# Optimization experiments

Measured on AMD Instinct MI355X. Metric: run time of the kernel, lower is better.

## Reference

```python
import jax, jax.numpy as jnp
import numpy as np

NUM_HEADS = 8
LN_EPS = 1e-6


def setup_inputs() -> dict:
    key = jax.random.key(0)
    ks = jax.random.split(key, 10)
    B, H, W, C = 4, 64, 64, 256
    s = 1.0 / np.sqrt(C)
    return {
        "x": jax.random.normal(ks[0], (B, H, W, C), jnp.float32),
        "Wq": jax.random.normal(ks[1], (C, C), jnp.float32) * s,
        "bq": jnp.zeros((C,), jnp.float32),
        "Wk": jax.random.normal(ks[2], (C, C), jnp.float32) * s,
        "bk": jnp.zeros((C,), jnp.float32),
        "Wv": jax.random.normal(ks[3], (C, C), jnp.float32) * s,
        "bv": jnp.zeros((C,), jnp.float32),
        "Wo": jax.random.normal(ks[4], (C, C), jnp.float32) * s,
        "bo": jnp.zeros((C,), jnp.float32),
        "gamma": jnp.ones((C,), jnp.float32),
        "beta": jnp.zeros((C,), jnp.float32),
    }


def reference(x, Wq, bq, Wk, bk, Wv, bv, Wo, bo, gamma, beta):
    B, H, W, C = x.shape
    N = H * W
    nh, dh = NUM_HEADS, C // NUM_HEADS
    xs = x.reshape(B, N, C)
    # torch Linear: y = x @ W.T + b
    q = (xs @ Wq.T + bq).reshape(B, N, nh, dh)
    k = (xs @ Wk.T + bk).reshape(B, N, nh, dh)
    v = (xs @ Wv.T + bv).reshape(B, N, nh, dh)
    residual = v.reshape(B, N, C)  # residual is V, per the original module
    # explicit attention (dropout on logits is identity in eval mode)
    scale = 1.0 / jnp.sqrt(jnp.asarray(dh, x.dtype))
    attn = jnp.einsum('bqhd,bkhd->bhqk', q, k) * scale  # [B, nh, N, N]
    probs = jax.nn.softmax(attn, axis=-1)
    out = jnp.einsum('bhqk,bkhd->bqhd', probs, v).reshape(B, N, C)
    out = out @ Wo.T + bo
    out = out + residual
    # LayerNorm over last dim, eps=1e-6
    mu = jnp.mean(out, axis=-1, keepdims=True)
    var = jnp.mean(jnp.square(out - mu), axis=-1, keepdims=True)
    out = (out - mu) * jax.lax.rsqrt(var + LN_EPS) * gamma + beta
    return out
```

## Files before the change

kernel.cpp:

```cpp
#include <hip/hip_runtime.h>
#include <hip/hip_bf16.h>
#include <math.h>

#define NHD 8
#define DH 32
#define CC 256
#define NTOK 4096
#define BATCH 4
#define MTOT 16384

typedef __attribute__((ext_vector_type(8))) short short8;
typedef __attribute__((ext_vector_type(4))) short s16x4;
typedef __attribute__((ext_vector_type(4))) float f32x4;
typedef __attribute__((ext_vector_type(16))) float f32x16;
typedef __attribute__((ext_vector_type(2))) unsigned int u32x2;

#if __has_builtin(__builtin_amdgcn_exp2f)
#define EXP2F __builtin_amdgcn_exp2f
#else
#define EXP2F exp2f
#endif

__device__ inline float bf2f(short s) {
    unsigned int u = ((unsigned int)(unsigned short)s) << 16;
    float f; __builtin_memcpy(&f, &u, 4); return f;
}
__device__ inline short f2bf(float f) {
    __hip_bfloat16 h = __float2bfloat16(f);
    unsigned short u; __builtin_memcpy(&u, &h, 2); return (short)u;
}
__device__ inline unsigned int pack2(float lo, float hi) {
    unsigned int a = (unsigned short)f2bf(lo);
    unsigned int b = (unsigned short)f2bf(hi);
    return a | (b << 16);
}
__device__ inline short8 mk8(unsigned int a, unsigned int b, unsigned int c, unsigned int d) {
    unsigned int t[4] = {a, b, c, d};
    short8 r; __builtin_memcpy(&r, t, 16); return r;
}

__global__ __launch_bounds__(256) void conv_x_kernel(const float* __restrict__ src,
                                                     short* __restrict__ dst, int n8) {
    int t = blockIdx.x * 256 + threadIdx.x;
    if (t >= n8) return;
    const f32x4* s4 = (const f32x4*)src;
    f32x4 a = s4[t * 2], b = s4[t * 2 + 1];
    short8 o;
    o[0] = f2bf(a[0]); o[1] = f2bf(a[1]); o[2] = f2bf(a[2]); o[3] = f2bf(a[3]);
    o[4] = f2bf(b[0]); o[5] = f2bf(b[1]); o[6] = f2bf(b[2]); o[7] = f2bf(b[3]);
    ((short8*)dst)[t] = o;
}

__global__ __launch_bounds__(256) void conv_w_kernel(const float* __restrict__ Wq,
                                                     const float* __restrict__ Wk,
                                                     const float* __restrict__ Wv,
                                                     const float* __restrict__ Wo,
                                                     short* __restrict__ dst) {
    int w = blockIdx.y;
    const float* src = (w == 0) ? Wq : (w == 1) ? Wk : (w == 2) ? Wv : Wo;
    int t = blockIdx.x * 256 + threadIdx.x;
    const f32x4* s4 = (const f32x4*)src;
    f32x4 a = s4[t * 2], b = s4[t * 2 + 1];
    short8 o;
    o[0] = f2bf(a[0]); o[1] = f2bf(a[1]); o[2] = f2bf(a[2]); o[3] = f2bf(a[3]);
    o[4] = f2bf(b[0]); o[5] = f2bf(b[1]); o[6] = f2bf(b[2]); o[7] = f2bf(b[3]);
    ((short8*)(dst + w * 65536))[t] = o;
}

__global__ __launch_bounds__(256) void qkv_kernel(const short* __restrict__ xb,
                                                  const short* __restrict__ Wb,
                                                  const float* __restrict__ bq,
                                                  const float* __restrict__ bk,
                                                  const float* __restrict__ bv,
                                                  short* __restrict__ Qb,
                                                  short* __restrict__ Kb,
                                                  short* __restrict__ Vt,
                                                  short* __restrict__ Vres) {
    int wsel = blockIdx.y;
    const short* W = Wb + wsel * 65536;
    int wave = threadIdx.x >> 6;
    int lane = threadIdx.x & 63;
    int lo = lane & 15, hi = lane >> 4;
    int m0 = blockIdx.x * 64 + wave * 16;

    f32x4 acc[16];
#pragma unroll
    for (int i = 0; i < 16; i++) acc[i] = (f32x4){0, 0, 0, 0};

    for (int ks = 0; ks < 8; ks++) {
        short8 a = *(const short8*)(xb + (m0 + lo) * 256 + ks * 32 + hi * 8);
#pragma unroll
        for (int nf = 0; nf < 16; nf++) {
            short8 b = *(const short8*)(W + (nf * 16 + lo) * 256 + ks * 32 + hi * 8);
            acc[nf] = __builtin_amdgcn_mfma_f32_16x16x32_bf16(a, b, acc[nf], 0, 0, 0);
        }
    }
    const float* bias = (wsel == 0) ? bq : (wsel == 1) ? bk : bv;
    const float qscale = 0.17677669529663687f * 1.4426950408889634f;
#pragma unroll
    for (int nf = 0; nf < 16; nf++) {
#pragma unroll
        for (int r = 0; r < 4; r++) {
            int m = m0 + hi * 4 + r;
            int c = nf * 16 + lo;
            float v = acc[nf][r] + bias[c];
            int bb = m >> 12, n = m & 4095;
            int h = c >> 5, d = c & 31;
            int bh = bb * 8 + h;
            if (wsel == 0)      Qb[(bh * 4096 + n) * 32 + d] = f2bf(v * qscale);
            else if (wsel == 1) Kb[(bh * 4096 + n) * 32 + d] = f2bf(v);
            else {
                short s = f2bf(v);
                Vt[(bh * 32 + d) * 4096 + n] = s;
                Vres[m * 256 + c] = s;
            }
        }
    }
}

__global__ __launch_bounds__(256, 4) void attn_kernel(const short* __restrict__ Qb,
                                                      const short* __restrict__ Kb,
                                                      const short* __restrict__ Vt,
                                                      short* __restrict__ O) {
    int bx = blockIdx.x;
    int bh = bx >> 5;
    int qb = bx & 31;
    int wave = threadIdx.x >> 6, lane = threadIdx.x & 63;
    int l31 = lane & 31, lh = lane >> 5;
    int q0 = qb * 128 + wave * 32;

    const short* Qrow = Qb + (bh * 4096 + q0 + l31) * 32;
    short8 bq0 = *(const short8*)(Qrow + lh * 8);
    short8 bq1 = *(const short8*)(Qrow + 16 + lh * 8);

    const short* Kbase = Kb + bh * 131072;
    const short* Vrow  = Vt + (bh * 32 + l31) * 4096;

    float mr = -1e30f, lr = 0.f;
    f32x16 oacc;
#pragma unroll
    for (int i = 0; i < 16; i++) oacc[i] = 0.f;

    for (int kv0 = 0; kv0 < 4096; kv0 += 32) {
        const short* Krow = Kbase + (kv0 + l31) * 32;
        short8 ak0 = *(const short8*)(Krow + lh * 8);
        short8 ak1 = *(const short8*)(Krow + 16 + lh * 8);
        short8 av0 = *(const short8*)(Vrow + kv0 + lh * 8);
        short8 av1 = *(const short8*)(Vrow + kv0 + 16 + lh * 8);

        f32x16 s;
#pragma unroll
        for (int i = 0; i < 16; i++) s[i] = 0.f;
        s = __builtin_amdgcn_mfma_f32_32x32x16_bf16(ak0, bq0, s, 0, 0, 0);
        s = __builtin_amdgcn_mfma_f32_32x32x16_bf16(ak1, bq1, s, 0, 0, 0);

        float m0_ = fmaxf(fmaxf(s[0], s[1]), fmaxf(s[2], s[3]));
        float m1_ = fmaxf(fmaxf(s[4], s[5]), fmaxf(s[6], s[7]));
        float m2_ = fmaxf(fmaxf(s[8], s[9]), fmaxf(s[10], s[11]));
        float m3_ = fmaxf(fmaxf(s[12], s[13]), fmaxf(s[14], s[15]));
        float mx = fmaxf(fmaxf(m0_, m1_), fmaxf(m2_, m3_));
        mx = fmaxf(mx, __shfl_xor(mx, 32, 64));

        float mnew = fmaxf(mr, mx);
        float al = EXP2F(mr - mnew);
        mr = mnew;

        float p[16];
#pragma unroll
        for (int i = 0; i < 16; i++) p[i] = EXP2F(s[i] - mnew);

        float r0 = (p[0] + p[1]) + (p[2] + p[3]);
        float r1 = (p[4] + p[5]) + (p[6] + p[7]);
        float r2 = (p[8] + p[9]) + (p[10] + p[11]);
        float r3 = (p[12] + p[13]) + (p[14] + p[15]);
        float rs = (r0 + r1) + (r2 + r3);
        rs += __shfl_xor(rs, 32, 64);

        lr = lr * al + rs;
#pragma unroll
        for (int i = 0; i < 16; i++) oacc[i] *= al;

        unsigned int w0 = pack2(p[0], p[1]),   w1 = pack2(p[2], p[3]);
        unsigned int w2 = pack2(p[4], p[5]),   w3 = pack2(p[6], p[7]);
        unsigned int w4 = pack2(p[8], p[9]),   w5 = pack2(p[10], p[11]);
        unsigned int w6 = pack2(p[12], p[13]), w7 = pack2(p[14], p[15]);
        short8 pb1, pb2;
#if __has_builtin(__builtin_amdgcn_permlane32_swap)
        u32x2 a0 = __builtin_amdgcn_permlane32_swap(w0, w2, false, false);
        u32x2 a1 = __builtin_amdgcn_permlane32_swap(w1, w3, false, false);
        u32x2 a2 = __builtin_amdgcn_permlane32_swap(w4, w6, false, false);
        u32x2 a3 = __builtin_amdgcn_permlane32_swap(w5, w7, false, false);
        pb1 = mk8(a0[0], a1[0], a0[1], a1[1]);
        pb2 = mk8(a2[0], a3[0], a2[1], a3[1]);
#else
        unsigned int x0 = __shfl_xor(w0, 32, 64), x1 = __shfl_xor(w1, 32, 64);
        unsigned int x2 = __shfl_xor(w2, 32, 64), x3 = __shfl_xor(w3, 32, 64);
        unsigned int x4 = __shfl_xor(w4, 32, 64), x5 = __shfl_xor(w5, 32, 64);
        unsigned int x6 = __shfl_xor(w6, 32, 64), x7 = __shfl_xor(w7, 32, 64);
        pb1 = mk8(lh ? x2 : w0, lh ? x3 : w1, lh ? w2 : x0, lh ? w3 : x1);
        pb2 = mk8(lh ? x6 : w4, lh ? x7 : w5, lh ? w6 : x4, lh ? w7 : x5);
#endif

        oacc = __builtin_amdgcn_mfma_f32_32x32x16_bf16(av0, pb1, oacc, 0, 0, 0);
        oacc = __builtin_amdgcn_mfma_f32_32x32x16_bf16(av1, pb2, oacc, 0, 0, 0);
    }

    float inv = 1.0f / lr;
    int token = (bh >> 3) * 4096 + q0 + l31;
    int c0 = (bh & 7) * 32 + 4 * lh;
#pragma unroll
    for (int j = 0; j < 4; j++) {
        s16x4 ow;
#pragma unroll
        for (int t = 0; t < 4; t++) ow[t] = f2bf(oacc[4 * j + t] * inv);
        *(s16x4*)(O + token * 256 + c0 + 8 * j) = ow;
    }
}

__global__ __launch_bounds__(256) void proj_ln_kernel(const short* __restrict__ O,
                                                      const short* __restrict__ Wob,
                                                      const float* __restrict__ bo,
                                                      const short* __restrict__ Vres,
                                                      const float* __restrict__ gamma,
                                                      const float* __restrict__ beta,
                                                      float* __restrict__ out) {
    int wave = threadIdx.x >> 6, lane = threadIdx.x & 63;
    int lo = lane & 15, hi = lane >> 4;
    int m0 = blockIdx.x * 64 + wave * 16;

    f32x4 acc[16];
#pragma unroll
    for (int i = 0; i < 16; i++) acc[i] = (f32x4){0, 0, 0, 0};

    for (int ks = 0; ks < 8; ks++) {
        short8 a = *(const short8*)(O + (m0 + lo) * 256 + ks * 32 + hi * 8);
#pragma unroll
        for (int nf = 0; nf < 16; nf++) {
            short8 b = *(const short8*)(Wob + (nf * 16 + lo) * 256 + ks * 32 + hi * 8);
            acc[nf] = __builtin_amdgcn_mfma_f32_16x16x32_bf16(a, b, acc[nf], 0, 0, 0);
        }
    }
#pragma unroll
    for (int nf = 0; nf < 16; nf++)
#pragma unroll
        for (int r = 0; r < 4; r++) {
            int m = m0 + hi * 4 + r;
            int c = nf * 16 + lo;
            acc[nf][r] += bo[c] + bf2f(Vres[m * 256 + c]);
        }
    float sum[4];
#pragma unroll
    for (int r = 0; r < 4; r++) {
        float t = 0.f;
#pragma unroll
        for (int nf = 0; nf < 16; nf++) t += acc[nf][r];
        sum[r] = t;
    }
#pragma unroll
    for (int d = 1; d < 16; d <<= 1)
#pragma unroll
        for (int r = 0; r < 4; r++) sum[r] += __shfl_xor(sum[r], d, 64);
    float mean[4];
#pragma unroll
    for (int r = 0; r < 4; r++) mean[r] = sum[r] * (1.0f / 256.0f);

    float ss[4];
#pragma unroll
    for (int r = 0; r < 4; r++) {
        float t = 0.f;
#pragma unroll
        for (int nf = 0; nf < 16; nf++) {
            float d_ = acc[nf][r] - mean[r];
            t += d_ * d_;
        }
        ss[r] = t;
    }
#pragma unroll
    for (int d = 1; d < 16; d <<= 1)
#pragma unroll
        for (int r = 0; r < 4; r++) ss[r] += __shfl_xor(ss[r], d, 64);
    float rstd[4];
#pragma unroll
    for (int r = 0; r < 4; r++) rstd[r] = rsqrtf(ss[r] * (1.0f / 256.0f) + 1e-6f);

#pragma unroll
    for (int nf = 0; nf < 16; nf++)
#pragma unroll
        for (int r = 0; r < 4; r++) {
            int m = m0 + hi * 4 + r;
            int c = nf * 16 + lo;
            out[m * 256 + c] = (acc[nf][r] - mean[r]) * rstd[r] * gamma[c] + beta[c];
        }
}

extern "C" void kernel_launch(void* const* d_in, const int* in_sizes, int n_in,
                              void* d_out, int out_size, void* d_ws, size_t ws_size,
                              hipStream_t stream) {
    const float* x     = (const float*)d_in[0];
    const float* Wq    = (const float*)d_in[1];
    const float* bq    = (const float*)d_in[2];
    const float* Wk    = (const float*)d_in[3];
    const float* bk    = (const float*)d_in[4];
    const float* Wv    = (const float*)d_in[5];
    const float* bv    = (const float*)d_in[6];
    const float* Wo    = (const float*)d_in[7];
    const float* bo    = (const float*)d_in[8];
    const float* gamma = (const float*)d_in[9];
    const float* beta  = (const float*)d_in[10];
    float* out = (float*)d_out;

    char* ws = (char*)d_ws;
    short* xb   = (short*)(ws);
    short* Qb   = (short*)(ws + 8388608);
    short* Kb   = (short*)(ws + 16777216);
    short* Vt   = (short*)(ws + 25165824);
    short* Vres = (short*)(ws + 33554432);
    short* Ob   = (short*)(ws + 41943040);
    short* Wb   = (short*)(ws + 50331648);
    short* Wob  = Wb + 3 * 65536;

    conv_x_kernel<<<2048, 256, 0, stream>>>(x, xb, 524288);
    conv_w_kernel<<<dim3(32, 4), 256, 0, stream>>>(Wq, Wk, Wv, Wo, Wb);
    qkv_kernel<<<dim3(256, 3), 256, 0, stream>>>(xb, Wb, bq, bk, bv, Qb, Kb, Vt, Vres);
    attn_kernel<<<1024, 256, 0, stream>>>(Qb, Kb, Vt, Ob);
    proj_ln_kernel<<<256, 256, 0, stream>>>(Ob, Wob, bo, Vres, gamma, beta, out);
}
```

Measured before the change: 348.5 us.

## Split attention KV range across wave pairs and merge partial softmax states

```diff
diff --git a/kernel.cpp b/kernel.cpp
--- a/kernel.cpp
+++ b/kernel.cpp
@@ -118,31 +118,36 @@
     }
 }
 
-__global__ __launch_bounds__(256, 4) void attn_kernel(const short* __restrict__ Qb,
+__global__ __launch_bounds__(256, 8) void attn_kernel(const short* __restrict__ Qb,
                                                       const short* __restrict__ Kb,
                                                       const short* __restrict__ Vt,
                                                       short* __restrict__ O) {
+    __shared__ float Osh[2][2][32][33];
+    __shared__ float Msh[2][2][32];
+    __shared__ float Lsh[2][2][32];
+
     int bx = blockIdx.x;
-    int bh = bx >> 5;
-    int qb = bx & 31;
+    int bh = bx >> 6;
+    int qbase = (bx & 63) * 64;
     int wave = threadIdx.x >> 6, lane = threadIdx.x & 63;
+    int tile = wave >> 1, half = wave & 1;
     int l31 = lane & 31, lh = lane >> 5;
-    int q0 = qb * 128 + wave * 32;
+    int q0 = qbase + tile * 32;
 
     const short* Qrow = Qb + (bh * 4096 + q0 + l31) * 32;
     short8 bq0 = *(const short8*)(Qrow + lh * 8);
     short8 bq1 = *(const short8*)(Qrow + 16 + lh * 8);
 
-    const short* Kbase = Kb + bh * 131072;
-    const short* Vrow  = Vt + (bh * 32 + l31) * 4096;
+    const short* Kh   = Kb + bh * 131072 + half * 65536;
+    const short* Vrow = Vt + (bh * 32 + l31) * 4096 + half * 2048;
 
     float mr = -1e30f, lr = 0.f;
     f32x16 oacc;
 #pragma unroll
     for (int i = 0; i < 16; i++) oacc[i] = 0.f;
 
-    for (int kv0 = 0; kv0 < 4096; kv0 += 32) {
-        const short* Krow = Kbase + (kv0 + l31) * 32;
+    for (int kv0 = 0; kv0 < 2048; kv0 += 32) {
+        const short* Krow = Kh + (kv0 + l31) * 32;
         short8 ak0 = *(const short8*)(Krow + lh * 8);
         short8 ak1 = *(const short8*)(Krow + 16 + lh * 8);
         short8 av0 = *(const short8*)(Vrow + kv0 + lh * 8);
@@ -154,20 +159,26 @@
         s = __builtin_amdgcn_mfma_f32_32x32x16_bf16(ak0, bq0, s, 0, 0, 0);
         s = __builtin_amdgcn_mfma_f32_32x32x16_bf16(ak1, bq1, s, 0, 0, 0);
 
-        float m0_ = fmaxf(fmaxf(s[0], s[1]), fmaxf(s[2], s[3]));
-        float m1_ = fmaxf(fmaxf(s[4], s[5]), fmaxf(s[6], s[7]));
-        float m2_ = fmaxf(fmaxf(s[8], s[9]), fmaxf(s[10], s[11]));
-        float m3_ = fmaxf(fmaxf(s[12], s[13]), fmaxf(s[14], s[15]));
-        float mx = fmaxf(fmaxf(m0_, m1_), fmaxf(m2_, m3_));
+        float t0 = fmaxf(fmaxf(s[0], s[1]), s[2]);
+        float t1 = fmaxf(fmaxf(s[3], s[4]), s[5]);
+        float t2 = fmaxf(fmaxf(s[6], s[7]), s[8]);
+        float t3 = fmaxf(fmaxf(s[9], s[10]), s[11]);
+        float t4 = fmaxf(fmaxf(s[12], s[13]), s[14]);
+        float mx = fmaxf(fmaxf(fmaxf(t0, t1), fmaxf(t2, t3)), fmaxf(t4, s[15]));
         mx = fmaxf(mx, __shfl_xor(mx, 32, 64));
 
-        float mnew = fmaxf(mr, mx);
-        float al = EXP2F(mr - mnew);
-        mr = mnew;
+        if (__any(mx > mr)) {
+            float mnew = fmaxf(mr, mx);
+            float al = EXP2F(mr - mnew);
+            mr = mnew;
+            lr *= al;
+#pragma unroll
+            for (int i = 0; i < 16; i++) oacc[i] *= al;
+        }
 
         float p[16];
 #pragma unroll
-        for (int i = 0; i < 16; i++) p[i] = EXP2F(s[i] - mnew);
+        for (int i = 0; i < 16; i++) p[i] = EXP2F(s[i] - mr);
 
         float r0 = (p[0] + p[1]) + (p[2] + p[3]);
         float r1 = (p[4] + p[5]) + (p[6] + p[7]);
@@ -175,10 +186,7 @@
         float r3 = (p[12] + p[13]) + (p[14] + p[15]);
         float rs = (r0 + r1) + (r2 + r3);
         rs += __shfl_xor(rs, 32, 64);
-
-        lr = lr * al + rs;
-#pragma unroll
-        for (int i = 0; i < 16; i++) oacc[i] *= al;
+        lr += rs;
 
         unsigned int w0 = pack2(p[0], p[1]),   w1 = pack2(p[2], p[3]);
         unsigned int w2 = pack2(p[4], p[5]),   w3 = pack2(p[6], p[7]);
@@ -205,16 +213,33 @@
         oacc = __builtin_amdgcn_mfma_f32_32x32x16_bf16(av1, pb2, oacc, 0, 0, 0);
     }
 
-    float inv = 1.0f / lr;
-    int token = (bh >> 3) * 4096 + q0 + l31;
-    int c0 = (bh & 7) * 32 + 4 * lh;
-#pragma unroll
-    for (int j = 0; j < 4; j++) {
-        s16x4 ow;
-#pragma unroll
-        for (int t = 0; t < 4; t++) ow[t] = f2bf(oacc[4 * j + t] * inv);
-        *(s16x4*)(O + token * 256 + c0 + 8 * j) = ow;
-    }
+#pragma unroll
+    for (int j = 0; j < 4; j++)
+#pragma unroll
+        for (int t = 0; t < 4; t++)
+            Osh[tile][half][l31][8 * j + 4 * lh + t] = oacc[4 * j + t];
+    if (lh == 0) { Msh[tile][half][l31] = mr; Lsh[tile][half][l31] = lr; }
+    __syncthreads();
+
+    int t = threadIdx.x;
+    int mt = t >> 7;
+    int idx = t & 127;
+    int q = idx >> 2;
+    int d0 = (idx & 3) * 8;
+    float m0 = Msh[mt][0][q], m1 = Msh[mt][1][q];
+    float l0 = Lsh[mt][0][q], l1 = Lsh[mt][1][q];
+    float mstar = fmaxf(m0, m1);
+    float e0 = EXP2F(m0 - mstar), e1 = EXP2F(m1 - mstar);
+    float inv = 1.0f / (l0 * e0 + l1 * e1);
+    int token = (bh >> 3) * 4096 + qbase + mt * 32 + q;
+    int c0 = (bh & 7) * 32 + d0;
+    short8 ow;
+#pragma unroll
+    for (int u = 0; u < 8; u++) {
+        float o = (Osh[mt][0][q][d0 + u] * e0 + Osh[mt][1][q][d0 + u] * e1) * inv;
+        ow[u] = f2bf(o);
+    }
+    *(short8*)(O + token * 256 + c0) = ow;
 }
 
 __global__ __launch_bounds__(256) void proj_ln_kernel(const short* __restrict__ O,
@@ -322,6 +347,6 @@
     conv_x_kernel<<<2048, 256, 0, stream>>>(x, xb, 524288);
     conv_w_kernel<<<dim3(32, 4), 256, 0, stream>>>(Wq, Wk, Wv, Wo, Wb);
     qkv_kernel<<<dim3(256, 3), 256, 0, stream>>>(xb, Wb, bq, bk, bv, Qb, Kb, Vt, Vres);
-    attn_kernel<<<1024, 256, 0, stream>>>(Qb, Kb, Vt, Ob);
+    attn_kernel<<<2048, 256, 0, stream>>>(Qb, Kb, Vt, Ob);
     proj_ln_kernel<<<256, 256, 0, stream>>>(Ob, Wob, bo, Vres, gamma, beta, out);
 }
```

Measured after the change: 400.3 us. +14.9%, slower.
